# Kernel optimization log

Hardware: AMD Instinct MI355X
Metric: run time of the kernel (lower is better)

Reference implementation:

```python
import jax, jax.numpy as jnp
import numpy as np

IN_DIM = 1024
OUT_DIM = 1024
NHEAD = 16
K = 9  # template(1032) - dim(1024) + 1


def _slinear(vec, template, conv_w, conv_b, lin_b):
    # Conv2d over template produces the [out_dim, in_dim] weight matrix.
    w = jax.lax.conv_general_dilated(
        template, conv_w, window_strides=(1, 1), padding='VALID',
        dimension_numbers=('NCHW', 'OIHW', 'NCHW'))  # [1,1,out_dim,in_dim]
    w = w[0, 0] + conv_b  # broadcast conv bias (scalar per out-channel)
    return vec @ w.T + lin_b  # F.linear(vec, w) + bias


def setup_inputs() -> dict:
    key = jax.random.key(0)
    ks = jax.random.split(key, 13)
    S, B = 2048, 2
    d = {
        'query': jax.random.normal(ks[0], (S, B, IN_DIM), jnp.float32),
        'key': jax.random.normal(ks[1], (S, B, IN_DIM), jnp.float32),
        'value': jax.random.normal(ks[2], (S, B, IN_DIM), jnp.float32),
        'template': jax.random.normal(ks[3], (1, 1, 1032, 1032), jnp.float32),
    }
    for i, name in enumerate(['wq', 'wk', 'wv']):
        d[name + '_cw'] = jax.random.normal(ks[4 + 3 * i], (1, 1, K, K), jnp.float32) * 0.05
        d[name + '_cb'] = jax.random.normal(ks[5 + 3 * i], (1,), jnp.float32) * 0.05
        d[name + '_b'] = jax.random.normal(ks[6 + 3 * i], (OUT_DIM,), jnp.float32) * 0.05
    return d


def reference(query, key, value, template,
              wq_cw, wq_cb, wq_b, wk_cw, wk_cb, wk_b, wv_cw, wv_cb, wv_b):
    q = _slinear(query, template, wq_cw, wq_cb, wq_b)
    k = _slinear(key, template, wk_cw, wk_cb, wk_b)
    v = _slinear(value, template, wv_cw, wv_cb, wv_b)
    S, B = q.shape[0], q.shape[1]
    h_dim = OUT_DIM // NHEAD
    scale = h_dim ** 0.5
    qh = q.reshape(S, B, NHEAD, h_dim)
    kh = k.reshape(S, B, NHEAD, h_dim)
    vh = v.reshape(S, B, NHEAD, h_dim)
    # batch_first=False path: scores then softmax over last dim
    scores = jnp.einsum('ibhd,jbhd->bhij', qh, kh) / scale  # [B,H,S,S]
    attn = jax.nn.softmax(scores, axis=-1)
    out = jnp.einsum('bhij,jbhd->ibhd', attn, vh).reshape(S, B, OUT_DIM)
    return out
```

## Files before the change

kernel.cpp:

```cpp
#include <hip/hip_runtime.h>
#include <math.h>

#define TDIM   1032
#define DIM    1024
#define SLEN   2048
#define BATCH  2
#define NROWS  (SLEN*BATCH)
#define NHEAD  16
#define HD     64

typedef unsigned short u16;
typedef short short8 __attribute__((ext_vector_type(8)));
typedef short bf16x4 __attribute__((ext_vector_type(4)));
typedef float f32x4  __attribute__((ext_vector_type(4)));

#define CSCALE 0.18033688011112042f

__device__ inline unsigned fbits(float x) {
    union { float f; unsigned u; } v; v.f = x; return v.u;
}
__device__ inline float asfloat(unsigned u) {
    union { unsigned u; float f; } v; v.u = u; return v.f;
}
__device__ inline u16 f2bf_rne(float x) {
    unsigned u = fbits(x);
    unsigned r = u + 0x7fffu + ((u >> 16) & 1u);
    return (u16)(r >> 16);
}
__device__ inline float bf2f(u16 b) { return asfloat(((unsigned)b) << 16); }
__device__ inline void dma16(const u16* g, u16* l) {
    __builtin_amdgcn_global_load_lds(
        (const __attribute__((address_space(1))) void*)g,
        (__attribute__((address_space(3))) void*)l, 16, 0, 0);
}

__global__ __launch_bounds__(256) void conv_weight_kernel(
    const float* __restrict__ tmpl,
    const float* __restrict__ cw0, const float* __restrict__ cb0,
    const float* __restrict__ cw1, const float* __restrict__ cb1,
    const float* __restrict__ cw2, const float* __restrict__ cb2,
    u16* __restrict__ Wh, u16* __restrict__ Wl)
{
    int t = blockIdx.z;
    const float* cw = (t == 0) ? cw0 : ((t == 1) ? cw1 : cw2);
    const float* cb = (t == 0) ? cb0 : ((t == 1) ? cb1 : cb2);
    __shared__ float scw[81];
    if (threadIdx.x < 81) scw[threadIdx.x] = cw[threadIdx.x];
    __syncthreads();
    int i = blockIdx.x * 256 + threadIdx.x;
    int o = blockIdx.y;
    float acc = cb[0];
    #pragma unroll
    for (int dy = 0; dy < 9; ++dy) {
        const float* trow = tmpl + (size_t)(o + dy) * TDIM + i;
        #pragma unroll
        for (int dx = 0; dx < 9; ++dx)
            acc = fmaf(scw[dy * 9 + dx], trow[dx], acc);
    }
    size_t idx = (size_t)t * DIM * DIM + (size_t)o * DIM + i;
    u16 h = f2bf_rne(acc);
    Wh[idx] = h;
    Wl[idx] = f2bf_rne(acc - bf2f(h));
}

__global__ __launch_bounds__(256, 3) void qkv_mfma_gemm(
    const float* __restrict__ x0, const float* __restrict__ x1,
    const float* __restrict__ x2,
    const u16* __restrict__ Whg, const u16* __restrict__ Wlg,
    const float* __restrict__ b0, const float* __restrict__ b1,
    const float* __restrict__ b2,
    u16* __restrict__ Qh, u16* __restrict__ Ql,
    u16* __restrict__ Kh, u16* __restrict__ Kl,
    u16* __restrict__ Vb)
{
    int t = blockIdx.z;
    const float* X    = (t == 0) ? x0 : ((t == 1) ? x1 : x2);
    const u16* Bh_g   = Whg + (size_t)t * DIM * DIM;
    const u16* Bl_g   = Wlg + (size_t)t * DIM * DIM;
    const float* bias = (t == 0) ? b0 : ((t == 1) ? b1 : b2);

    __shared__ __align__(16) u16 lds[16384];
    u16* sAh = lds;
    u16* sAl = lds + 4096;
    u16* sBh = lds + 8192;
    u16* sBl = lds + 12288;

    int tid = threadIdx.x;
    int w = tid >> 6, lane = tid & 63;
    int c = lane & 15, quad = lane >> 4;
    int m0 = blockIdx.y * 128, n0 = blockIdx.x * 128;
    int mh = (w >> 1) * 64, nh = (w & 1) * 64;

    int arow = w * 32 + (lane & 31);
    int acol = (lane >> 5) * 16;
    const float* aptr = X + (size_t)(m0 + arow) * DIM + acol;

    int srow = lane >> 2, sgr = lane & 3;

    f32x4 acc[4][4];
    #pragma unroll
    for (int i = 0; i < 4; ++i)
        #pragma unroll
        for (int j = 0; j < 4; ++j)
            #pragma unroll
            for (int r = 0; r < 4; ++r) acc[i][j][r] = 0.0f;

    float bias_v[4];
    #pragma unroll
    for (int tn = 0; tn < 4; ++tn) bias_v[tn] = bias[n0 + nh + tn * 16 + c];

    float4 xa[4];
    #pragma unroll
    for (int i = 0; i < 2; ++i) {
        int rb = w * 32 + i * 16;
        const u16* gh = Bh_g + (size_t)(n0 + rb + srow) * DIM + sgr * 8;
        const u16* gl = Bl_g + (size_t)(n0 + rb + srow) * DIM + sgr * 8;
        dma16(gh, sBh + rb * 32);
        dma16(gl, sBl + rb * 32);
    }
    #pragma unroll
    for (int j = 0; j < 4; ++j) xa[j] = *(const float4*)(aptr + j * 4);

    for (int it = 0; it < 32; ++it) {
        #pragma unroll
        for (int g = 0; g < 2; ++g) {
            float v[8] = { xa[2*g].x, xa[2*g].y, xa[2*g].z, xa[2*g].w,
                           xa[2*g+1].x, xa[2*g+1].y, xa[2*g+1].z, xa[2*g+1].w };
            short8 hv, lv;
            #pragma unroll
            for (int e = 0; e < 8; ++e) {
                unsigned u = fbits(v[e]);
                hv[e] = (short)(u >> 16);
                float l = v[e] - asfloat(u & 0xffff0000u);
                lv[e] = (short)(fbits(l) >> 16);
            }
            *(short8*)(sAh + arow * 32 + acol + g * 8) = hv;
            *(short8*)(sAl + arow * 32 + acol + g * 8) = lv;
        }
        __syncthreads();

        short8 ah[4], al[4], bh[4], bl[4];
        #pragma unroll
        for (int tt = 0; tt < 4; ++tt) {
            int mi = (mh + tt * 16 + c) * 32 + quad * 8;
            ah[tt] = *(short8*)(sAh + mi);
            al[tt] = *(short8*)(sAl + mi);
            int ni = (nh + tt * 16 + c) * 32 + quad * 8;
            bh[tt] = *(short8*)(sBh + ni);
            bl[tt] = *(short8*)(sBl + ni);
        }
        __syncthreads();

        if (it < 31) {
            int kg = (it + 1) * 4;
            #pragma unroll
            for (int i = 0; i < 2; ++i) {
                int rb = w * 32 + i * 16;
                const u16* gh = Bh_g + (size_t)(n0 + rb + srow) * DIM + (kg + sgr) * 8;
                const u16* gl = Bl_g + (size_t)(n0 + rb + srow) * DIM + (kg + sgr) * 8;
                dma16(gh, sBh + rb * 32);
                dma16(gl, sBl + rb * 32);
            }
            #pragma unroll
            for (int j = 0; j < 4; ++j)
                xa[j] = *(const float4*)(aptr + (it + 1) * 32 + j * 4);
        }

        #pragma unroll
        for (int tm = 0; tm < 4; ++tm)
            #pragma unroll
            for (int tn = 0; tn < 4; ++tn) {
                acc[tm][tn] = __builtin_amdgcn_mfma_f32_16x16x32_bf16(
                    ah[tm], bh[tn], acc[tm][tn], 0, 0, 0);
                acc[tm][tn] = __builtin_amdgcn_mfma_f32_16x16x32_bf16(
                    ah[tm], bl[tn], acc[tm][tn], 0, 0, 0);
                acc[tm][tn] = __builtin_amdgcn_mfma_f32_16x16x32_bf16(
                    al[tm], bh[tn], acc[tm][tn], 0, 0, 0);
            }
    }

    if (t < 2) {
        u16* Yh = (t == 0) ? Qh : Kh;
        u16* Yl = (t == 0) ? Ql : Kl;
        float qs = (t == 0) ? CSCALE : 1.0f;
        #pragma unroll
        for (int tm = 0; tm < 4; ++tm)
            #pragma unroll
            for (int r = 0; r < 4; ++r) {
                int m = m0 + mh + tm * 16 + quad * 4 + r;
                #pragma unroll
                for (int tn = 0; tn < 4; ++tn) {
                    int n = n0 + nh + tn * 16 + c;
                    float o = (acc[tm][tn][r] + bias_v[tn]) * qs;
                    unsigned bo = fbits(o);
                    Yh[(size_t)m * DIM + n] = (u16)(bo >> 16);
                    float l = o - asfloat(bo & 0xffff0000u);
                    Yl[(size_t)m * DIM + n] = (u16)(fbits(l) >> 16);
                }
            }
    } else {
        #pragma unroll
        for (int tm = 0; tm < 4; ++tm)
            #pragma unroll
            for (int r = 0; r < 4; ++r) {
                int m = m0 + mh + tm * 16 + quad * 4 + r;
                #pragma unroll
                for (int tn = 0; tn < 4; ++tn) {
                    int n = n0 + nh + tn * 16 + c;
                    Vb[(size_t)m * DIM + n] =
                        (u16)(fbits(acc[tm][tn][r] + bias_v[tn]) >> 16);
                }
            }
    }
}

__global__ __launch_bounds__(256) void vt_kernel(
    const u16* __restrict__ Vb, u16* __restrict__ Vt)
{
    int b = blockIdx.z, h = blockIdx.y, s0 = blockIdx.x * 64;
    __shared__ __align__(16) u16 tile[64][80];
    int tid = threadIdx.x;
    int sl = tid >> 2, d0 = (tid & 3) * 16;
    const u16* src = Vb + (size_t)((s0 + sl) * BATCH + b) * DIM + h * HD + d0;
    short8 v0 = *(const short8*)src;
    short8 v1 = *(const short8*)(src + 8);
    #pragma unroll
    for (int j = 0; j < 8; ++j) {
        tile[d0 + j][sl] = (u16)v0[j];
        tile[d0 + 8 + j][sl] = (u16)v1[j];
    }
    __syncthreads();
    int d = tid >> 2, sc0 = (tid & 3) * 16;
    u16* dst = Vt + (size_t)((b * NHEAD + h) * HD + d) * SLEN + s0 + sc0;
    *(short8*)dst = *(const short8*)&tile[d][sc0];
    *(short8*)(dst + 8) = *(const short8*)&tile[d][sc0 + 8];
}

__global__ __launch_bounds__(256) void attn_mfma_kernel(
    const u16* __restrict__ Qh, const u16* __restrict__ Ql,
    const u16* __restrict__ Kh, const u16* __restrict__ Kl,
    const u16* __restrict__ Vt, float* __restrict__ out)
{
    int b = blockIdx.z, h = blockIdx.y;
    int q0 = blockIdx.x * 128;
    int tid = threadIdx.x;
    int w = tid >> 6, lane = tid & 63;
    int c = lane & 15, quad = lane >> 4;

    __shared__ __align__(16) u16 sbuf[2][3][4096];
    __shared__ __align__(16) u16 sP[4][2048];

    short8 qhf[2][2], qlf[2][2];
    #pragma unroll
    for (int u = 0; u < 2; ++u) {
        int s = q0 + w * 32 + u * 16 + c;
        size_t base = (size_t)(s * BATCH + b) * DIM + h * HD + quad * 8;
        qhf[u][0] = *(const short8*)(Qh + base);
        qhf[u][1] = *(const short8*)(Qh + base + 32);
        qlf[u][0] = *(const short8*)(Ql + base);
        qlf[u][1] = *(const short8*)(Ql + base + 32);
    }

    f32x4 acc[2][4];
    #pragma unroll
    for (int u = 0; u < 2; ++u)
        #pragma unroll
        for (int i = 0; i < 4; ++i)
            #pragma unroll
            for (int r = 0; r < 4; ++r) acc[u][i][r] = 0.0f;
    float m_run[2] = {-1e38f, -1e38f}, l_run[2] = {0.0f, 0.0f};

    int r3 = lane >> 3, c3 = lane & 7;
    int sw = c3 ^ r3;
    const size_t bhofs = (size_t)(b * NHEAD + h) * HD;

    #define ISSUE_DMA(n0v, bufv) do {                                          \
        _Pragma("unroll")                                                      \
        for (int j = 0; j < 2; ++j) {                                          \
            int i_ = 2 * w + j;                                                \
            int row_ = i_ * 8 + r3;                                            \
            size_t gk = (size_t)(((n0v) + row_) * BATCH + b) * DIM + h * HD + sw * 8; \
            dma16(Kh + gk, &sbuf[bufv][0][i_ * 512]);                          \
            dma16(Kl + gk, &sbuf[bufv][1][i_ * 512]);                          \
            size_t gv = (bhofs + row_) * SLEN + (n0v) + sw * 8;                \
            dma16(Vt + gv, &sbuf[bufv][2][i_ * 512]);                          \
        }                                                                      \
    } while (0)

    ISSUE_DMA(0, 0);

    for (int it = 0; it < 32; ++it) {
        int cur = it & 1;
        __syncthreads();
        if (it < 31) ISSUE_DMA((it + 1) * 64, cur ^ 1);

        const u16* bKh = sbuf[cur][0];
        const u16* bKl = sbuf[cur][1];
        const u16* bVt = sbuf[cur][2];

        f32x4 sc[2][4];
        #pragma unroll
        for (int ct = 0; ct < 4; ++ct) {
            int row = ct * 16 + c, rw = row & 7;
            int kb = row * 64;
            short8 kh0 = *(const short8*)(bKh + kb + ((quad ^ rw) * 8));
            short8 kh1 = *(const short8*)(bKh + kb + (((4 + quad) ^ rw) * 8));
            short8 kl0 = *(const short8*)(bKl + kb + ((quad ^ rw) * 8));
            short8 kl1 = *(const short8*)(bKl + kb + (((4 + quad) ^ rw) * 8));
            #pragma unroll
            for (int u = 0; u < 2; ++u) {
                f32x4 s = {0.0f, 0.0f, 0.0f, 0.0f};
                s = __builtin_amdgcn_mfma_f32_16x16x32_bf16(kh0, qhf[u][0], s, 0, 0, 0);
                s = __builtin_amdgcn_mfma_f32_16x16x32_bf16(kh1, qhf[u][1], s, 0, 0, 0);
                s = __builtin_amdgcn_mfma_f32_16x16x32_bf16(kh0, qlf[u][0], s, 0, 0, 0);
                s = __builtin_amdgcn_mfma_f32_16x16x32_bf16(kh1, qlf[u][1], s, 0, 0, 0);
                s = __builtin_amdgcn_mfma_f32_16x16x32_bf16(kl0, qhf[u][0], s, 0, 0, 0);
                s = __builtin_amdgcn_mfma_f32_16x16x32_bf16(kl1, qhf[u][1], s, 0, 0, 0);
                sc[u][ct] = s;
            }
        }

        u16* wp = sP[w];
        #pragma unroll
        for (int u = 0; u < 2; ++u) {
            float pm = sc[u][0][0];
            #pragma unroll
            for (int ct = 0; ct < 4; ++ct)
                #pragma unroll
                for (int r = 0; r < 4; ++r)
                    pm = fmaxf(pm, sc[u][ct][r]);
            pm = fmaxf(pm, __shfl_xor(pm, 16));
            pm = fmaxf(pm, __shfl_xor(pm, 32));
            float mnew = fmaxf(m_run[u], pm);
            float al = exp2f(m_run[u] - mnew);
            m_run[u] = mnew;
            float ps = 0.0f;
            int prow = (u * 16 + c) * 64;
            #pragma unroll
            for (int ct = 0; ct < 4; ++ct) {
                bf16x4 pk;
                #pragma unroll
                for (int r = 0; r < 4; ++r) {
                    float p = exp2f(sc[u][ct][r] - mnew);
                    ps += p;
                    pk[r] = (short)(fbits(p) >> 16);
                }
                int phys = (ct * 2 + (quad >> 1)) ^ (c & 7);
                *(bf16x4*)(wp + prow + phys * 8 + (quad & 1) * 4) = pk;
            }
            ps += __shfl_xor(ps, 16);
            ps += __shfl_xor(ps, 32);
            l_run[u] = l_run[u] * al + ps;

            float alr[4];
            #pragma unroll
            for (int r = 0; r < 4; ++r)
                alr[r] = __shfl(al, (lane & 48) | (quad * 4 + r));
            #pragma unroll
            for (int ctd = 0; ctd < 4; ++ctd)
                #pragma unroll
                for (int r = 0; r < 4; ++r) acc[u][ctd][r] *= alr[r];
        }

        short8 pf[2][2];
        #pragma unroll
        for (int u = 0; u < 2; ++u) {
            int prow = (u * 16 + c) * 64, rw = c & 7;
            pf[u][0] = *(const short8*)(wp + prow + ((quad ^ rw) * 8));
            pf[u][1] = *(const short8*)(wp + prow + (((4 + quad) ^ rw) * 8));
        }
        #pragma unroll
        for (int ctd = 0; ctd < 4; ++ctd) {
            int vrow = ctd * 16 + c, vrw = vrow & 7;
            int vb = vrow * 64;
            short8 v0 = *(const short8*)(bVt + vb + ((quad ^ vrw) * 8));
            short8 v1 = *(const short8*)(bVt + vb + (((4 + quad) ^ vrw) * 8));
            #pragma unroll
            for (int u = 0; u < 2; ++u) {
                acc[u][ctd] = __builtin_amdgcn_mfma_f32_16x16x32_bf16(
                    pf[u][0], v0, acc[u][ctd], 0, 0, 0);
                acc[u][ctd] = __builtin_amdgcn_mfma_f32_16x16x32_bf16(
                    pf[u][1], v1, acc[u][ctd], 0, 0, 0);
            }
        }
    }
    #undef ISSUE_DMA

    #pragma unroll
    for (int u = 0; u < 2; ++u) {
        float rl[4];
        #pragma unroll
        for (int r = 0; r < 4; ++r)
            rl[r] = 1.0f / __shfl(l_run[u], (lane & 48) | (quad * 4 + r));
        #pragma unroll
        for (int ctd = 0; ctd < 4; ++ctd)
            #pragma unroll
            for (int r = 0; r < 4; ++r) {
                int s = q0 + w * 32 + u * 16 + quad * 4 + r;
                out[(size_t)(s * BATCH + b) * DIM + h * HD + ctd * 16 + c] =
                    acc[u][ctd][r] * rl[r];
            }
    }
}

extern "C" void kernel_launch(void* const* d_in, const int* in_sizes, int n_in,
                              void* d_out, int out_size, void* d_ws, size_t ws_size,
                              hipStream_t stream)
{
    const float* query = (const float*)d_in[0];
    const float* key_  = (const float*)d_in[1];
    const float* value = (const float*)d_in[2];
    const float* tmpl  = (const float*)d_in[3];
    const float* wq_cw = (const float*)d_in[4];
    const float* wq_cb = (const float*)d_in[5];
    const float* wq_b  = (const float*)d_in[6];
    const float* wk_cw = (const float*)d_in[7];
    const float* wk_cb = (const float*)d_in[8];
    const float* wk_b  = (const float*)d_in[9];
    const float* wv_cw = (const float*)d_in[10];
    const float* wv_cb = (const float*)d_in[11];
    const float* wv_b  = (const float*)d_in[12];

    char* ws = (char*)d_ws;
    u16* Wh = (u16*)(ws);
    u16* Wl = (u16*)(ws + 6291456);
    u16* Qh = (u16*)(ws + 12582912);
    u16* Ql = (u16*)(ws + 20971520);
    u16* Kh = (u16*)(ws + 29360128);
    u16* Kl = (u16*)(ws + 37748736);
    u16* Vb = (u16*)(ws + 46137344);
    u16* Vt = (u16*)(ws + 54525952);
    float* out = (float*)d_out;

    conv_weight_kernel<<<dim3(DIM / 256, DIM, 3), 256, 0, stream>>>(
        tmpl, wq_cw, wq_cb, wk_cw, wk_cb, wv_cw, wv_cb, Wh, Wl);

    qkv_mfma_gemm<<<dim3(DIM / 128, NROWS / 128, 3), 256, 0, stream>>>(
        query, key_, value, Wh, Wl, wq_b, wk_b, wv_b, Qh, Ql, Kh, Kl, Vb);

    vt_kernel<<<dim3(SLEN / 64, NHEAD, BATCH), 256, 0, stream>>>(Vb, Vt);

    attn_mfma_kernel<<<dim3(SLEN / 128, NHEAD, BATCH), 256, 0, stream>>>(
        Qh, Ql, Kh, Kl, Vt, out);
}
```

Baseline: 338.9 us.

## Register-resident P via shuffles, skip-rescale, XCD swizzles, and 4-row conv blocking

The conv weight kernel now computes four output rows per thread, reusing each loaded template row across overlapping filter taps to cut redundant loads. The QKV GEMM and attention kernels remap block indices so that neighbouring blocks land on the same XCD for better L2 locality. The attention kernel drops the LDS round trip for the probability tile and instead builds the MFMA operand fragments directly with lane shuffles. It also skips the output rescale when the running max is unchanged across the wave, raises wave priority around MFMA bursts, and adds an occupancy hint of three blocks per CU. These changes add many shuffles and some divergence checks, and the occupancy hint may cause register spills.

```diff
diff --git a/kernel.cpp b/kernel.cpp
--- a/kernel.cpp
+++ b/kernel.cpp
@@ -48,19 +48,32 @@
     if (threadIdx.x < 81) scw[threadIdx.x] = cw[threadIdx.x];
     __syncthreads();
     int i = blockIdx.x * 256 + threadIdx.x;
-    int o = blockIdx.y;
-    float acc = cb[0];
-    #pragma unroll
-    for (int dy = 0; dy < 9; ++dy) {
-        const float* trow = tmpl + (size_t)(o + dy) * TDIM + i;
-        #pragma unroll
-        for (int dx = 0; dx < 9; ++dx)
-            acc = fmaf(scw[dy * 9 + dx], trow[dx], acc);
-    }
-    size_t idx = (size_t)t * DIM * DIM + (size_t)o * DIM + i;
-    u16 h = f2bf_rne(acc);
-    Wh[idx] = h;
-    Wl[idx] = f2bf_rne(acc - bf2f(h));
+    int o4 = blockIdx.y * 4;
+    float cbv = cb[0];
+    float acc[4] = {cbv, cbv, cbv, cbv};
+    #pragma unroll
+    for (int ry = 0; ry < 12; ++ry) {
+        const float* trow = tmpl + (size_t)(o4 + ry) * TDIM + i;
+        float tv[9];
+        #pragma unroll
+        for (int dx = 0; dx < 9; ++dx) tv[dx] = trow[dx];
+        #pragma unroll
+        for (int oo = 0; oo < 4; ++oo) {
+            int dy = ry - oo;
+            if (dy >= 0 && dy <= 8) {
+                #pragma unroll
+                for (int dx = 0; dx < 9; ++dx)
+                    acc[oo] = fmaf(scw[dy * 9 + dx], tv[dx], acc[oo]);
+            }
+        }
+    }
+    #pragma unroll
+    for (int oo = 0; oo < 4; ++oo) {
+        size_t idx = (size_t)t * DIM * DIM + (size_t)(o4 + oo) * DIM + i;
+        u16 h = f2bf_rne(acc[oo]);
+        Wh[idx] = h;
+        Wl[idx] = f2bf_rne(acc[oo] - bf2f(h));
+    }
 }
 
 __global__ __launch_bounds__(256, 3) void qkv_mfma_gemm(
@@ -73,7 +86,12 @@
     u16* __restrict__ Kh, u16* __restrict__ Kl,
     u16* __restrict__ Vb)
 {
-    int t = blockIdx.z;
+    unsigned flat = blockIdx.x + 8u * blockIdx.y + 256u * blockIdx.z;
+    unsigned swz = (flat & 7u) * 96u + (flat >> 3);
+    int t = swz >> 8;
+    int n0 = (swz & 7u) * 128;
+    int m0 = ((swz >> 3) & 31u) * 128;
+
     const float* X    = (t == 0) ? x0 : ((t == 1) ? x1 : x2);
     const u16* Bh_g   = Whg + (size_t)t * DIM * DIM;
     const u16* Bl_g   = Wlg + (size_t)t * DIM * DIM;
@@ -88,7 +106,6 @@
     int tid = threadIdx.x;
     int w = tid >> 6, lane = tid & 63;
     int c = lane & 15, quad = lane >> 4;
-    int m0 = blockIdx.y * 128, n0 = blockIdx.x * 128;
     int mh = (w >> 1) * 64, nh = (w & 1) * 64;
 
     int arow = w * 32 + (lane & 31);
@@ -236,19 +253,22 @@
     *(short8*)(dst + 8) = *(const short8*)&tile[d][sc0 + 8];
 }
 
-__global__ __launch_bounds__(256) void attn_mfma_kernel(
+__global__ __launch_bounds__(256, 3) void attn_mfma_kernel(
     const u16* __restrict__ Qh, const u16* __restrict__ Ql,
     const u16* __restrict__ Kh, const u16* __restrict__ Kl,
     const u16* __restrict__ Vt, float* __restrict__ out)
 {
-    int b = blockIdx.z, h = blockIdx.y;
-    int q0 = blockIdx.x * 128;
+    unsigned flat = blockIdx.x + 16u * blockIdx.y + 256u * blockIdx.z;
+    unsigned swz = (flat & 7u) * 64u + (flat >> 3);
+    int q0 = (swz & 15u) * 128;
+    int h = (swz >> 4) & 15u;
+    int b = swz >> 8;
+
     int tid = threadIdx.x;
     int w = tid >> 6, lane = tid & 63;
     int c = lane & 15, quad = lane >> 4;
 
     __shared__ __align__(16) u16 sbuf[2][3][4096];
-    __shared__ __align__(16) u16 sP[4][2048];
 
     short8 qhf[2][2], qlf[2][2];
     #pragma unroll
@@ -307,6 +327,7 @@
             short8 kh1 = *(const short8*)(bKh + kb + (((4 + quad) ^ rw) * 8));
             short8 kl0 = *(const short8*)(bKl + kb + ((quad ^ rw) * 8));
             short8 kl1 = *(const short8*)(bKl + kb + (((4 + quad) ^ rw) * 8));
+            __builtin_amdgcn_s_setprio(1);
             #pragma unroll
             for (int u = 0; u < 2; ++u) {
                 f32x4 s = {0.0f, 0.0f, 0.0f, 0.0f};
@@ -318,9 +339,10 @@
                 s = __builtin_amdgcn_mfma_f32_16x16x32_bf16(kl1, qhf[u][1], s, 0, 0, 0);
                 sc[u][ct] = s;
             }
-        }
-
-        u16* wp = sP[w];
+            __builtin_amdgcn_s_setprio(0);
+        }
+
+        short8 pf[2][2];
         #pragma unroll
         for (int u = 0; u < 2; ++u) {
             float pm = sc[u][0][0];
@@ -332,49 +354,70 @@
             pm = fmaxf(pm, __shfl_xor(pm, 16));
             pm = fmaxf(pm, __shfl_xor(pm, 32));
             float mnew = fmaxf(m_run[u], pm);
-            float al = exp2f(m_run[u] - mnew);
+            bool noresc = __all(pm <= m_run[u]);
+            if (!noresc) {
+                float al = exp2f(m_run[u] - mnew);
+                float alr[4];
+                #pragma unroll
+                for (int r = 0; r < 4; ++r)
+                    alr[r] = __shfl(al, (lane & 48) | (quad * 4 + r));
+                #pragma unroll
+                for (int ctd = 0; ctd < 4; ++ctd)
+                    #pragma unroll
+                    for (int r = 0; r < 4; ++r) acc[u][ctd][r] *= alr[r];
+                l_run[u] *= al;
+            }
             m_run[u] = mnew;
+
             float ps = 0.0f;
-            int prow = (u * 16 + c) * 64;
+            unsigned pw[8];
             #pragma unroll
             for (int ct = 0; ct < 4; ++ct) {
-                bf16x4 pk;
-                #pragma unroll
-                for (int r = 0; r < 4; ++r) {
-                    float p = exp2f(sc[u][ct][r] - mnew);
-                    ps += p;
-                    pk[r] = (short)(fbits(p) >> 16);
-                }
-                int phys = (ct * 2 + (quad >> 1)) ^ (c & 7);
-                *(bf16x4*)(wp + prow + phys * 8 + (quad & 1) * 4) = pk;
+                float p0 = exp2f(sc[u][ct][0] - mnew);
+                float p1 = exp2f(sc[u][ct][1] - mnew);
+                float p2 = exp2f(sc[u][ct][2] - mnew);
+                float p3 = exp2f(sc[u][ct][3] - mnew);
+                ps += (p0 + p1) + (p2 + p3);
+                pw[2*ct]   = (fbits(p0) >> 16) | (fbits(p1) & 0xffff0000u);
+                pw[2*ct+1] = (fbits(p2) >> 16) | (fbits(p3) & 0xffff0000u);
             }
             ps += __shfl_xor(ps, 16);
             ps += __shfl_xor(ps, 32);
-            l_run[u] = l_run[u] * al + ps;
-
-            float alr[4];
-            #pragma unroll
-            for (int r = 0; r < 4; ++r)
-                alr[r] = __shfl(al, (lane & 48) | (quad * 4 + r));
-            #pragma unroll
-            for (int ctd = 0; ctd < 4; ++ctd)
-                #pragma unroll
-                for (int r = 0; r < 4; ++r) acc[u][ctd][r] *= alr[r];
-        }
-
-        short8 pf[2][2];
-        #pragma unroll
-        for (int u = 0; u < 2; ++u) {
-            int prow = (u * 16 + c) * 64, rw = c & 7;
-            pf[u][0] = *(const short8*)(wp + prow + ((quad ^ rw) * 8));
-            pf[u][1] = *(const short8*)(wp + prow + (((4 + quad) ^ rw) * 8));
-        }
+            l_run[u] += ps;
+
+            int sl0 = c + ((quad & 1) << 5);
+            int sl1 = sl0 + 16;
+            int sel = quad >> 1;
+            union W8 { unsigned wv[4]; short8 s8; } f0, f1;
+            {
+                unsigned a0 = __shfl(pw[0], sl0), a1 = __shfl(pw[2], sl0);
+                f0.wv[0] = sel ? a1 : a0;
+                unsigned b0 = __shfl(pw[1], sl0), b1 = __shfl(pw[3], sl0);
+                f0.wv[1] = sel ? b1 : b0;
+                unsigned c0 = __shfl(pw[0], sl1), c1 = __shfl(pw[2], sl1);
+                f0.wv[2] = sel ? c1 : c0;
+                unsigned d0 = __shfl(pw[1], sl1), d1 = __shfl(pw[3], sl1);
+                f0.wv[3] = sel ? d1 : d0;
+                unsigned e0 = __shfl(pw[4], sl0), e1 = __shfl(pw[6], sl0);
+                f1.wv[0] = sel ? e1 : e0;
+                unsigned g0 = __shfl(pw[5], sl0), g1 = __shfl(pw[7], sl0);
+                f1.wv[1] = sel ? g1 : g0;
+                unsigned h0 = __shfl(pw[4], sl1), h1 = __shfl(pw[6], sl1);
+                f1.wv[2] = sel ? h1 : h0;
+                unsigned i0 = __shfl(pw[5], sl1), i1 = __shfl(pw[7], sl1);
+                f1.wv[3] = sel ? i1 : i0;
+            }
+            pf[u][0] = f0.s8;
+            pf[u][1] = f1.s8;
+        }
+
         #pragma unroll
         for (int ctd = 0; ctd < 4; ++ctd) {
             int vrow = ctd * 16 + c, vrw = vrow & 7;
             int vb = vrow * 64;
             short8 v0 = *(const short8*)(bVt + vb + ((quad ^ vrw) * 8));
             short8 v1 = *(const short8*)(bVt + vb + (((4 + quad) ^ vrw) * 8));
+            __builtin_amdgcn_s_setprio(1);
             #pragma unroll
             for (int u = 0; u < 2; ++u) {
                 acc[u][ctd] = __builtin_amdgcn_mfma_f32_16x16x32_bf16(
@@ -382,6 +425,7 @@
                 acc[u][ctd] = __builtin_amdgcn_mfma_f32_16x16x32_bf16(
                     pf[u][1], v1, acc[u][ctd], 0, 0, 0);
             }
+            __builtin_amdgcn_s_setprio(0);
         }
     }
     #undef ISSUE_DMA
@@ -432,7 +476,7 @@
     u16* Vt = (u16*)(ws + 54525952);
     float* out = (float*)d_out;
 
-    conv_weight_kernel<<<dim3(DIM / 256, DIM, 3), 256, 0, stream>>>(
+    conv_weight_kernel<<<dim3(DIM / 256, DIM / 4, 3), 256, 0, stream>>>(
         tmpl, wq_cw, wq_cb, wk_cw, wk_cb, wv_cw, wv_cb, Wh, Wl);
 
     qkv_mfma_gemm<<<dim3(DIM / 128, NROWS / 128, 3), 256, 0, stream>>>(
```

Measured after the change: 321.7 us. 1.05x faster.
